# Kernel optimization log

Measured on AMD Instinct MI355X. Metric: run time of the kernel, lower is better.

Reference implementation:

```python
import jax, jax.numpy as jnp
import numpy as np
import math

M = 0.65
S = 64.0
WEIGHT = 0.003
COS_M = math.cos(M)
SIN_M = math.sin(M)
THRESHOLD = math.cos(math.pi - M)
MM = math.sin(math.pi - M) * M

B, D, C = 512, 512, 100000


def l2_norm(x, axis):
    return x / jnp.linalg.norm(x, ord=2, axis=axis, keepdims=True)


def setup_inputs() -> dict:
    key = jax.random.key(0)
    k1, k2, k3 = jax.random.split(key, 3)
    embbedings = jax.random.normal(k1, (B, D), dtype=jnp.float32)
    kernel = 0.01 * jax.random.normal(k2, (D, C), dtype=jnp.float32)  # Parameter init std=0.01
    t = jnp.zeros((1,), dtype=jnp.float32)  # running buffer
    label = jax.random.randint(k3, (B,), 0, C, dtype=jnp.int64)
    return {"embbedings": embbedings, "kernel": kernel, "t": t, "label": label}


def reference(embbedings, kernel, t, label):
    emb = l2_norm(embbedings, axis=1)          # [B, D]
    kernel_norm = l2_norm(kernel, axis=0)      # [D, C]
    cos_theta = jnp.clip(emb @ kernel_norm, -1.0, 1.0)  # [B, C]
    origin_cos = jax.lax.stop_gradient(cos_theta)       # torch: clone under no_grad

    rows = jnp.arange(cos_theta.shape[0])
    target_logit = cos_theta[rows, label][:, None]       # [B, 1]
    sin_theta = jnp.sqrt(1.0 - target_logit ** 2)
    cos_theta_m = target_logit * COS_M - sin_theta * SIN_M

    mask = cos_theta > cos_theta_m                       # [B, C]
    final_target_logit = jnp.where(target_logit > THRESHOLD,
                                   cos_theta_m, target_logit - MM)

    # buffer update (no_grad), used immediately for hard-example reweighting
    t_new = jax.lax.stop_gradient(target_logit.mean()) * 0.01 + 0.99 * t  # [1]

    ct = jnp.where(mask, cos_theta * (t_new + cos_theta), cos_theta)
    ct = ct.at[rows, label].set(final_target_logit[:, 0])  # scatter_ on dim 1
    output = ct * S  # dropout with p=0 is identity

    # angular center loss; center is detached (no_grad clone) in torch
    center = jax.lax.stop_gradient(kernel.T)[label]       # [B, D]
    c_norm = l2_norm(center, axis=1)
    cos_theta_center = jnp.clip(jnp.sum(emb * c_norm, axis=1), -1.0, 1.0)
    center_loss = jnp.mean(jnp.arccos(cos_theta_center) ** 1.5)

    return output, origin_cos * S, S * WEIGHT * center_loss
```

## Files before the change

### kernel.cpp

```cpp
#include <hip/hip_runtime.h>
#include <hip/hip_bf16.h>
#include <stdint.h>

#define B_M 512
#define D_K 512
#define C_N 100000
#define S_SCALE 64.0f
#define W_LOSS 0.003f
#define COS_M_C 0.79608379854905604f
#define SIN_M_C 0.60518640573603957f
#define THRESH_C (-0.79608379854905604f)
#define MM_C 0.39337116372842573f

typedef __bf16 bf16x8 __attribute__((ext_vector_type(8)));
typedef float f32x4 __attribute__((ext_vector_type(4)));

typedef const __attribute__((address_space(1))) unsigned char* gptr_t;
typedef __attribute__((address_space(3))) unsigned char* sptr_t;

__device__ __forceinline__ unsigned short f2bf(float f) {
  __bf16 h = (__bf16)f;
  return __builtin_bit_cast(unsigned short, h);
}

__global__ __launch_bounds__(256) void prep_kernel(
    const float* __restrict__ emb, const float* __restrict__ Kg,
    const int* __restrict__ label, unsigned char* __restrict__ wsA,
    float* __restrict__ tl)
{
  int b = blockIdx.x, t = threadIdx.x;
  __shared__ float row[512];
  __shared__ float r1[256], r2[256];

  float2 v = ((const float2*)(emb + (size_t)b * 512))[t];
  r1[t] = v.x * v.x + v.y * v.y;
  __syncthreads();
  for (int s = 128; s > 0; s >>= 1) {
    if (t < s) r1[t] += r1[t + s];
    __syncthreads();
  }
  float inv = 1.0f / sqrtf(r1[0]);
  float e0 = v.x * inv, e1 = v.y * inv;
  row[2 * t] = e0;
  row[2 * t + 1] = e1;

  {
    int mhalf = b >> 8, lrow = b & 255;
    int kk = t >> 5;
    int byte_in = (4 * (t & 31)) ^ ((lrow & 7) << 4);
    ushort2 h;
    h.x = f2bf(e0);
    h.y = f2bf(e1);
    *(ushort2*)(wsA + (size_t)(mhalf * 8 + kk) * 32768 + lrow * 128 + byte_in) = h;
  }
  __syncthreads();

  int lab = label[b];
  const float* kc = Kg + lab;
  float dot = 0.f, csq = 0.f;
  for (int d = t; d < 512; d += 256) {
    float kv = kc[(size_t)d * C_N];
    dot += row[d] * kv;
    csq += kv * kv;
  }
  r1[t] = dot;
  r2[t] = csq;
  __syncthreads();
  for (int s = 128; s > 0; s >>= 1) {
    if (t < s) { r1[t] += r1[t + s]; r2[t] += r2[t + s]; }
    __syncthreads();
  }
  if (t == 0) {
    float tlv = r1[0] / sqrtf(r2[0]);
    tl[b] = fminf(1.f, fmaxf(-1.f, tlv));
  }
}

__global__ __launch_bounds__(512) void finalize_kernel(
    const float* __restrict__ tl, const float* __restrict__ t_in,
    float* __restrict__ ctm, float* __restrict__ ftl,
    float* __restrict__ tnew, float* __restrict__ out3)
{
  int t = threadIdx.x;
  float v = tl[t];
  __shared__ float r1[512], r2[512];
  float ac = acosf(v);
  r1[t] = v;
  r2[t] = ac * sqrtf(ac);
  __syncthreads();
  for (int s = 256; s > 0; s >>= 1) {
    if (t < s) { r1[t] += r1[t + s]; r2[t] += r2[t + s]; }
    __syncthreads();
  }
  if (t == 0) {
    tnew[0] = 0.99f * t_in[0] + 0.01f * (r1[0] / 512.0f);
    out3[0] = S_SCALE * W_LOSS * (r2[0] / 512.0f);
  }
  float st = sqrtf(fmaxf(0.f, 1.f - v * v));
  float cm = v * COS_M_C - st * SIN_M_C;
  ctm[t] = cm;
  ftl[t] = (v > THRESH_C) ? cm : (v - MM_C);
}

#define LDS_TOTAL 46336

__global__ __launch_bounds__(512, 4) void gemm_kernel(
    const float* __restrict__ Kg, const unsigned char* __restrict__ wsA,
    const float* __restrict__ ctm_g, const float* __restrict__ ftl_g,
    const int* __restrict__ label, const float* __restrict__ tnew_g,
    float* __restrict__ out1, float* __restrict__ out2)
{
  __shared__ __align__(16) unsigned char smem[LDS_TOTAL];

  int t = threadIdx.x;
  int lane = t & 63, wv = t >> 6;
  int wm = wv >> 2, wn = wv & 3;
  int kq = lane >> 4, lr = lane & 15;

  int bid = blockIdx.x;
  {
    int xcd = bid & 7, seq = bid >> 3;
    bid = (xcd < 6 ? xcd * 391 : 6 * 391 + (xcd - 6) * 390) + seq;
  }
  int pid = bid >> 1, mhalf = bid & 1;
  long c0 = (long)pid * 64;

  int c = t & 63, kseg = t >> 6;
  bool binb = (c0 + c) < C_N;
  const float* Bcol = Kg + c0 + c + (size_t)kseg * 8 * C_N;

  f32x4 acc[8] = {};
  float csq = 0.f;
  float bf[8];

  const unsigned char* wsTile = wsA + (size_t)mhalf * (8 * 32768);
  unsigned char* smemA = smem;
  unsigned char* smemB = smem + 32768;
  unsigned char* browB = smemB + c * 128;

#define LOAD_B(j)                                                            \
  {                                                                          \
    const float* src = Bcol + (size_t)((j) * 64) * C_N;                      \
    _Pragma("unroll") for (int i = 0; i < 8; ++i)                            \
        bf[i] = binb ? src[(size_t)i * C_N] : 0.f;                           \
  }

#define WRITE_B()                                                            \
  {                                                                          \
    _Pragma("unroll") for (int i = 0; i < 8; ++i) csq += bf[i] * bf[i];      \
    union { unsigned short u[8]; uint4 q; } pk;                              \
    _Pragma("unroll") for (int i = 0; i < 8; ++i) pk.u[i] = f2bf(bf[i]);     \
    *(uint4*)(browB + ((kseg * 16) ^ ((c & 7) << 4))) = pk.q;                \
  }

  LOAD_B(0);

#pragma unroll
  for (int kkt = 0; kkt < 8; ++kkt) {
    __syncthreads();
    const unsigned char* tA = wsTile + (size_t)kkt * 32768;
#pragma unroll
    for (int i = 0; i < 4; ++i) {
      int off = wv * 4096 + i * 1024;
      __builtin_amdgcn_global_load_lds((gptr_t)(tA + off + lane * 16),
                                       (sptr_t)(smemA + off), 16, 0, 0);
    }
    __builtin_amdgcn_sched_barrier(0);
    WRITE_B();
    if (kkt < 7) LOAD_B(kkt + 1);
    __builtin_amdgcn_sched_barrier(0);
    if (kkt < 7) {
      asm volatile("s_waitcnt vmcnt(8)" ::: "memory");
    } else {
      asm volatile("s_waitcnt vmcnt(0)" ::: "memory");
    }
    __builtin_amdgcn_sched_barrier(0);
    __syncthreads();

#pragma unroll
    for (int ks = 0; ks < 2; ++ks) {
      int kb = ks * 64 + kq * 16;
      int n = wn * 16 + lr;
      bf16x8 bfr = *(const bf16x8*)(smemB + n * 128 + (kb ^ ((n & 7) << 4)));
#pragma unroll
      for (int mf = 0; mf < 8; ++mf) {
        int m = wm * 128 + mf * 16 + lr;
        bf16x8 afr = *(const bf16x8*)(smemA + m * 128 + (kb ^ ((m & 7) << 4)));
        acc[mf] = __builtin_amdgcn_mfma_f32_16x16x32_bf16(afr, bfr, acc[mf], 0, 0, 0);
      }
    }
  }

  float* colpart = (float*)(smem + 40960);
  float* invn    = (float*)(smem + 43008);
  float* ctm_s   = (float*)(smem + 43264);
  float* ftl_s   = (float*)(smem + 44288);
  int*   lab_s   = (int*)  (smem + 45312);
  colpart[t] = csq;
  if (t < 256) {
    ctm_s[t] = ctm_g[mhalf * 256 + t];
    ftl_s[t] = ftl_g[mhalf * 256 + t];
    lab_s[t] = label[mhalf * 256 + t];
  }
  __syncthreads();
  if (t < 64) {
    float s = 0.f;
#pragma unroll
    for (int g = 0; g < 8; ++g) s += colpart[g * 64 + t];
    invn[t] = 1.0f / sqrtf(fmaxf(s, 1e-30f));
  }
  __syncthreads();
  float tn = tnew_g[0];

  for (int q = 0; q < 2; ++q) {
    if (wm == q) {
#pragma unroll
      for (int mf = 0; mf < 8; ++mf) {
#pragma unroll
        for (int j = 0; j < 4; ++j) {
          int row = mf * 16 + kq * 4 + j;
          int col = wn * 16 + lr;
          *(float*)(smem + row * 256 + ((col * 4) ^ (((row >> 2) & 3) << 6))) =
              acc[mf][j];
        }
      }
    }
    __syncthreads();
#pragma unroll
    for (int rr = 0; rr < 4; ++rr) {
      int row = rr * 32 + (t >> 4);
      int cb = (t & 15) * 4;
      f32x4 v = *(const f32x4*)(smem + row * 256 + ((cb * 4) ^ (((row >> 2) & 3) << 6)));
      long cgs = c0 + cb;
      if (cgs < C_N) {
        int lrow = q * 128 + row;
        float cm = ctm_s[lrow], fl = ftl_s[lrow];
        int lb = lab_s[lrow];
        f32x4 iv = *(const f32x4*)(invn + cb);
        f32x4 o1v, o2v;
#pragma unroll
        for (int jj = 0; jj < 4; ++jj) {
          float cosv = fminf(1.f, fmaxf(-1.f, v[jj] * iv[jj]));
          o2v[jj] = cosv * S_SCALE;
          float ct = (cosv > cm) ? cosv * (tn + cosv) : cosv;
          if (lb == (int)(cgs + jj)) ct = fl;
          o1v[jj] = ct * S_SCALE;
        }
        size_t idx = (size_t)(mhalf * 256 + lrow) * C_N + cgs;
        __builtin_nontemporal_store(o1v, (f32x4*)(out1 + idx));
        __builtin_nontemporal_store(o2v, (f32x4*)(out2 + idx));
      }
    }
    __syncthreads();
  }
#undef LOAD_B
#undef WRITE_B
}

extern "C" void kernel_launch(void* const* d_in, const int* in_sizes, int n_in,
                              void* d_out, int out_size, void* d_ws, size_t ws_size,
                              hipStream_t stream)
{
  const float* emb   = (const float*)d_in[0];
  const float* Kg    = (const float*)d_in[1];
  const float* t_in  = (const float*)d_in[2];
  const int*   label = (const int*)d_in[3];

  float* out1 = (float*)d_out;
  float* out2 = out1 + (size_t)B_M * C_N;
  float* out3 = out1 + 2 * (size_t)B_M * C_N;

  unsigned char* wsA = (unsigned char*)d_ws;
  float* tl   = (float*)((unsigned char*)d_ws + 524288);
  float* ctm  = tl + 512;
  float* ftl  = ctm + 512;
  float* tnew = ftl + 512;

  prep_kernel<<<512, 256, 0, stream>>>(emb, Kg, label, wsA, tl);
  finalize_kernel<<<1, 512, 0, stream>>>(tl, t_in, ctm, ftl, tnew, out3);
  int nb = 2 * 1563;
  gemm_kernel<<<nb, 512, 0, stream>>>(Kg, wsA, ctm, ftl, label, tnew, out1, out2);
}
```

Measured before the change: 147.7 us.

## Double-buffer A tiles in LDS and prefetch B two stages ahead

The GEMM main loop now keeps two LDS buffers for the A tile, so the next tile's global_load_lds runs while the MFMAs work on the current one. B register staging is also doubled, so loads run two k-steps ahead. This hides global load latency behind compute. In exchange, LDS grows to 72KB and launch bounds drop from 4 to 2 blocks per CU, which lowers occupancy and adds an extra barrier per iteration.

Result: faster. 142.7 us (median of 2 runs) (-3.4%).

```diff
diff --git a/kernel.cpp b/kernel.cpp
--- a/kernel.cpp
+++ b/kernel.cpp
@@ -102,9 +102,9 @@
   ftl[t] = (v > THRESH_C) ? cm : (v - MM_C);
 }
 
-#define LDS_TOTAL 46336
-
-__global__ __launch_bounds__(512, 4) void gemm_kernel(
+#define LDS_TOTAL 73728
+
+__global__ __launch_bounds__(512, 2) void gemm_kernel(
     const float* __restrict__ Kg, const unsigned char* __restrict__ wsA,
     const float* __restrict__ ctm_g, const float* __restrict__ ftl_g,
     const int* __restrict__ label, const float* __restrict__ tnew_g,
@@ -131,52 +131,64 @@
 
   f32x4 acc[8] = {};
   float csq = 0.f;
-  float bf[8];
+  float bf0[8], bf1[8];
 
   const unsigned char* wsTile = wsA + (size_t)mhalf * (8 * 32768);
-  unsigned char* smemA = smem;
-  unsigned char* smemB = smem + 32768;
+  unsigned char* smemB = smem + 65536;
   unsigned char* browB = smemB + c * 128;
 
-#define LOAD_B(j)                                                            \
+#define LOAD_B(dst, j)                                                       \
   {                                                                          \
     const float* src = Bcol + (size_t)((j) * 64) * C_N;                      \
     _Pragma("unroll") for (int i = 0; i < 8; ++i)                            \
-        bf[i] = binb ? src[(size_t)i * C_N] : 0.f;                           \
-  }
-
-#define WRITE_B()                                                            \
+        dst[i] = binb ? src[(size_t)i * C_N] : 0.f;                          \
+  }
+
+#define WRITE_B(src)                                                         \
   {                                                                          \
-    _Pragma("unroll") for (int i = 0; i < 8; ++i) csq += bf[i] * bf[i];      \
+    _Pragma("unroll") for (int i = 0; i < 8; ++i) csq += src[i] * src[i];    \
     union { unsigned short u[8]; uint4 q; } pk;                              \
-    _Pragma("unroll") for (int i = 0; i < 8; ++i) pk.u[i] = f2bf(bf[i]);     \
+    _Pragma("unroll") for (int i = 0; i < 8; ++i) pk.u[i] = f2bf(src[i]);    \
     *(uint4*)(browB + ((kseg * 16) ^ ((c & 7) << 4))) = pk.q;                \
   }
 
-  LOAD_B(0);
-
-#pragma unroll
-  for (int kkt = 0; kkt < 8; ++kkt) {
-    __syncthreads();
-    const unsigned char* tA = wsTile + (size_t)kkt * 32768;
+  {
 #pragma unroll
     for (int i = 0; i < 4; ++i) {
       int off = wv * 4096 + i * 1024;
-      __builtin_amdgcn_global_load_lds((gptr_t)(tA + off + lane * 16),
-                                       (sptr_t)(smemA + off), 16, 0, 0);
-    }
-    __builtin_amdgcn_sched_barrier(0);
-    WRITE_B();
-    if (kkt < 7) LOAD_B(kkt + 1);
-    __builtin_amdgcn_sched_barrier(0);
+      __builtin_amdgcn_global_load_lds((gptr_t)(wsTile + off + lane * 16),
+                                       (sptr_t)(smem + off), 16, 0, 0);
+    }
+    __builtin_amdgcn_sched_barrier(0);
+    LOAD_B(bf0, 0);
+    __builtin_amdgcn_sched_barrier(0);
+    LOAD_B(bf1, 1);
+    __builtin_amdgcn_sched_barrier(0);
+    asm volatile("s_waitcnt vmcnt(8)" ::: "memory");
+    __builtin_amdgcn_sched_barrier(0);
+    WRITE_B(bf0);
+    __syncthreads();
+  }
+
+#pragma unroll
+  for (int kkt = 0; kkt < 8; ++kkt) {
+    int cur = kkt & 1;
     if (kkt < 7) {
-      asm volatile("s_waitcnt vmcnt(8)" ::: "memory");
-    } else {
-      asm volatile("s_waitcnt vmcnt(0)" ::: "memory");
-    }
-    __builtin_amdgcn_sched_barrier(0);
-    __syncthreads();
-
+      const unsigned char* tA = wsTile + (size_t)(kkt + 1) * 32768;
+#pragma unroll
+      for (int i = 0; i < 4; ++i) {
+        int off = wv * 4096 + i * 1024;
+        __builtin_amdgcn_global_load_lds((gptr_t)(tA + off + lane * 16),
+                                         (sptr_t)(smem + (cur ^ 1) * 32768 + off), 16, 0, 0);
+      }
+      __builtin_amdgcn_sched_barrier(0);
+    }
+    if (kkt < 6) {
+      if (kkt & 1) { LOAD_B(bf1, kkt + 2); } else { LOAD_B(bf0, kkt + 2); }
+      __builtin_amdgcn_sched_barrier(0);
+    }
+
+    const unsigned char* Ab = smem + cur * 32768;
 #pragma unroll
     for (int ks = 0; ks < 2; ++ks) {
       int kb = ks * 64 + kq * 16;
@@ -185,17 +197,30 @@
 #pragma unroll
       for (int mf = 0; mf < 8; ++mf) {
         int m = wm * 128 + mf * 16 + lr;
-        bf16x8 afr = *(const bf16x8*)(smemA + m * 128 + (kb ^ ((m & 7) << 4)));
+        bf16x8 afr = *(const bf16x8*)(Ab + m * 128 + (kb ^ ((m & 7) << 4)));
         acc[mf] = __builtin_amdgcn_mfma_f32_16x16x32_bf16(afr, bfr, acc[mf], 0, 0, 0);
       }
     }
-  }
-
-  float* colpart = (float*)(smem + 40960);
-  float* invn    = (float*)(smem + 43008);
-  float* ctm_s   = (float*)(smem + 43264);
-  float* ftl_s   = (float*)(smem + 44288);
-  int*   lab_s   = (int*)  (smem + 45312);
+
+    if (kkt < 6) {
+      asm volatile("s_waitcnt vmcnt(8)" ::: "memory");
+    } else {
+      asm volatile("s_waitcnt vmcnt(0)" ::: "memory");
+    }
+    __builtin_amdgcn_sched_barrier(0);
+    __syncthreads();
+
+    if (kkt < 7) {
+      if (kkt & 1) { WRITE_B(bf0); } else { WRITE_B(bf1); }
+      __syncthreads();
+    }
+  }
+
+  float* colpart = (float*)(smem + 65536);
+  float* invn    = (float*)(smem + 67584);
+  float* ctm_s   = (float*)(smem + 67840);
+  float* ftl_s   = (float*)(smem + 68864);
+  int*   lab_s   = (int*)  (smem + 69888);
   colpart[t] = csq;
   if (t < 256) {
     ctm_s[t] = ctm_g[mhalf * 256 + t];
```
